# Kernel optimization log

Hardware: AMD Instinct MI355X
Metric: run time of the kernel (lower is better)

Reference implementation:

```python
import math
import jax, jax.numpy as jnp
import numpy as np

EPS_NORM = 1e-6
EPS_COS = 1e-6


def setup_inputs() -> dict:
    key = jax.random.key(0)
    ks = jax.random.split(key, 6)
    B, C, T, H, W = 2, 768, 8, 24, 24
    d_head = 64
    nh = C // d_head  # 12
    x = jax.random.normal(ks[0], (B, C, T, H, W), jnp.float32)
    pos = jax.random.uniform(ks[1], (B, H, W, 2), jnp.float32)
    cond = jax.random.normal(ks[2], (B, C), jnp.float32)
    # NOTE: original zero-inits norm.linear and out_proj; we use small random
    # weights so the reference exercises the full math path.
    norm_w = jax.random.normal(ks[3], (C, C), jnp.float32) * 0.02
    qkv_w = jax.random.normal(ks[4], (3 * C, C), jnp.float32) * (1.0 / math.sqrt(C))
    scale = jnp.full((nh,), 10.0, jnp.float32)
    out_w = jax.random.normal(ks[5], (C, C), jnp.float32) * 0.02
    # AxialRoPE freqs buffer, exactly as in torch:
    dim = d_head // 2
    n = nh * dim // 4
    lf = np.linspace(math.log(math.pi), math.log(10.0 * math.pi), n + 1)[:-1]
    freqs = jnp.asarray(np.exp(lf).reshape(dim // 4, nh).T, jnp.float32)  # [nh, d_head//8]
    return dict(x=x, pos=pos, cond=cond, norm_w=norm_w, qkv_w=qkv_w,
                scale=scale, out_w=out_w, freqs=freqs)


def reference(x, pos, cond, norm_w, qkv_w, scale, out_w, freqs):
    B, C, T, H, W = x.shape
    nh = freqs.shape[0]
    e = C // nh
    s = H * W
    n = B * T
    skip = x

    # b c t h w -> (b t) h w c
    xr = jnp.transpose(x, (0, 2, 3, 4, 1)).reshape(n, H, W, C)
    # cond: b c -> (b t) c
    condr = jnp.repeat(cond, T, axis=0)

    # AdaRMSNorm
    cs = condr @ norm_w.T + 1.0  # [n, C]
    ms = jnp.mean(xr.astype(jnp.float32) ** 2, axis=-1, keepdims=True)
    xn = (xr * (cs[:, None, None, :] * jax.lax.rsqrt(ms + EPS_NORM))).astype(x.dtype)

    # QKV projection
    qkv = xn @ qkv_w.T  # [n, H, W, 3C]
    qkv = qkv.reshape(n, s, 3, nh, e)
    q = jnp.transpose(qkv[:, :, 0], (0, 2, 1, 3))  # [n, nh, s, e]
    k = jnp.transpose(qkv[:, :, 1], (0, 2, 1, 3))
    v = jnp.transpose(qkv[:, :, 2], (0, 2, 1, 3))

    # cosine-sim QK rescale (per-head learned scale)
    sq = jnp.sqrt(scale)[:, None, None]  # [nh,1,1]
    q = q * (sq * jax.lax.rsqrt(jnp.sum(q ** 2, axis=-1, keepdims=True) + EPS_COS))
    k = k * (sq * jax.lax.rsqrt(jnp.sum(k ** 2, axis=-1, keepdims=True) + EPS_COS))

    # axial RoPE: theta [B, s, nh, 2*dth] -> repeat over T -> [n, nh, s, d]
    posf = pos.reshape(B, s, 2)
    th = posf[:, :, 0, None, None] * freqs  # [B, s, nh, dth]
    tw = posf[:, :, 1, None, None] * freqs
    theta = jnp.concatenate([th, tw], axis=-1)
    theta = jnp.repeat(theta, T, axis=0)
    theta = jnp.transpose(theta, (0, 2, 1, 3))  # [n, nh, s, d]
    cos_t, sin_t = jnp.cos(theta), jnp.sin(theta)
    d = theta.shape[-1]

    def rot(t):
        t1, t2, rest = t[..., :d], t[..., d:2 * d], t[..., 2 * d:]
        return jnp.concatenate([t1 * cos_t - t2 * sin_t,
                                t2 * cos_t + t1 * sin_t, rest], axis=-1)

    q = rot(q)
    k = rot(k)

    # SDPA with scale=1.0
    attn = jax.nn.softmax(jnp.einsum('bhqe,bhke->bhqk', q, k), axis=-1)
    o = jnp.einsum('bhqk,bhke->bhqe', attn, v)  # [n, nh, s, e]

    # n nh (h w) e -> n h w (nh e)
    o = jnp.transpose(o, (0, 2, 1, 3)).reshape(n, H, W, C)
    o = o @ out_w.T
    # (b t) h w c -> b c t h w
    o = o.reshape(B, T, H, W, C).transpose(0, 4, 1, 2, 3)
    return o + skip
```

## Files before the change

kernel.cpp:

```cpp
#include <hip/hip_runtime.h>
#include <hip/hip_bf16.h>

#define CDIM 768
#define NHEAD 12
#define EDIM 64
#define TDIM 8
#define SDIM 576
#define NROW 16
#define MDIM 9216
#define QKVN 2304

typedef __attribute__((ext_vector_type(4))) float f32x4;
typedef __bf16 bf16x8 __attribute__((ext_vector_type(8)));
typedef unsigned short u16;
typedef __attribute__((ext_vector_type(8))) unsigned short u16x8;

__device__ inline float bf2f(u16 u) {
  union { unsigned int i; float f; } x; x.i = ((unsigned int)u) << 16; return x.f;
}
__device__ inline u16 f2bf(float f) {
  union { float f; unsigned int i; } x; x.f = f;
  unsigned int i = x.i;
  return (u16)((i + 0x7FFFu + ((i >> 16) & 1u)) >> 16);
}
__device__ inline unsigned cvt_pk_bf16(float lo, float hi) {
  unsigned r;
  asm("v_cvt_pk_bf16_f32 %0, %1, %2" : "=v"(r) : "v"(lo), "v"(hi));
  return r;
}

__global__ __launch_bounds__(256) void prep_kernel(const float* __restrict__ qkv_w,
                                                   u16* __restrict__ wq,
                                                   const float* __restrict__ out_w,
                                                   u16* __restrict__ wo,
                                                   const float* __restrict__ cond,
                                                   const float* __restrict__ nw,
                                                   float* __restrict__ cs,
                                                   const float* __restrict__ pos,
                                                   const float* __restrict__ freqs,
                                                   float2* __restrict__ trig) {
  int bid = blockIdx.x;
  int tid = threadIdx.x;
  if (bid < 1728) {
    int i = bid * 256 + tid;
    float4 v = *(const float4*)(qkv_w + (size_t)i * 4);
    u16* d = wq + (size_t)i * 4;
    d[0] = f2bf(v.x); d[1] = f2bf(v.y); d[2] = f2bf(v.z); d[3] = f2bf(v.w);
  } else if (bid < 2304) {
    int i = (bid - 1728) * 256 + tid;
    float4 v = *(const float4*)(out_w + (size_t)i * 4);
    u16* d = wo + (size_t)i * 4;
    d[0] = f2bf(v.x); d[1] = f2bf(v.y); d[2] = f2bf(v.z); d[3] = f2bf(v.w);
  } else if (bid < 2310) {
    int idx = (bid - 2304) * 256 + tid;
    int b = idx / CDIM, c = idx - b * CDIM;
    const float* cr = cond + (size_t)b * CDIM;
    const float* wr = nw + (size_t)c * CDIM;
    float s = 1.0f;
    for (int j = 0; j < CDIM; j += 4) {
      float4 a = *(const float4*)(cr + j);
      float4 w = *(const float4*)(wr + j);
      s = fmaf(a.x, w.x, s); s = fmaf(a.y, w.y, s);
      s = fmaf(a.z, w.z, s); s = fmaf(a.w, w.w, s);
    }
    cs[idx] = s;
  } else {
    int idx = (bid - 2310) * 256 + tid;
    int j = idx & 15;
    int h = (idx >> 4) % NHEAD;
    int bs = idx / (16 * NHEAD);
    float p = pos[(size_t)bs * 2 + (j >> 3)];
    float th = p * freqs[h * 8 + (j & 7)];
    float sn, cn;
    __sincosf(th, &sn, &cn);
    trig[idx] = make_float2(cn, sn);
  }
}

__global__ __launch_bounds__(256) void norm_kernel(const float* __restrict__ x,
                                                   const float* __restrict__ cs,
                                                   u16* __restrict__ xn) {
  __shared__ float xs[16][772];
  __shared__ float red[16][17];
  __shared__ float rfac[16];
  int n = blockIdx.y;
  int hw0 = blockIdx.x * 16;
  int b = n >> 3, t = n & 7;
  int tx = threadIdx.x, ty = threadIdx.y;
  const float* xb = x + ((size_t)b * CDIM * TDIM + t) * SDIM;
  float acc = 0.0f;
  for (int c = ty; c < CDIM; c += 16) {
    float v = xb[(size_t)c * (TDIM * SDIM) + hw0 + tx];
    xs[tx][c] = v;
    acc = fmaf(v, v, acc);
  }
  red[ty][tx] = acc;
  __syncthreads();
  if (ty == 0) {
    float s = 0.0f;
    #pragma unroll
    for (int j = 0; j < 16; j++) s += red[j][tx];
    rfac[tx] = rsqrtf(s * (1.0f / (float)CDIM) + 1e-6f);
  }
  __syncthreads();
  const float* csb = cs + (size_t)b * CDIM;
  int flat = ty * 16 + tx;
  #pragma unroll
  for (int i = 0; i < 6; i++) {
    int idx = i * 256 + flat;
    int row = idx / 96;
    int cseg = idx - row * 96;
    int c0 = cseg * 8;
    float rf = rfac[row];
    float4 a0 = *(const float4*)&xs[row][c0];
    float4 a1 = *(const float4*)&xs[row][c0 + 4];
    float4 w0 = *(const float4*)(csb + c0);
    float4 w1 = *(const float4*)(csb + c0 + 4);
    u16x8 ov;
    ov[0] = f2bf(a0.x * w0.x * rf); ov[1] = f2bf(a0.y * w0.y * rf);
    ov[2] = f2bf(a0.z * w0.z * rf); ov[3] = f2bf(a0.w * w0.w * rf);
    ov[4] = f2bf(a1.x * w1.x * rf); ov[5] = f2bf(a1.y * w1.y * rf);
    ov[6] = f2bf(a1.z * w1.z * rf); ov[7] = f2bf(a1.w * w1.w * rf);
    *(u16x8*)(xn + ((size_t)n * SDIM + hw0 + row) * CDIM + c0) = ov;
  }
}

__device__ __forceinline__ void gemm_bt_lds(const u16* __restrict__ A,
                                            const u16* __restrict__ B,
                                            int K, int m0, int n0, int tid,
                                            u16* ldsA, u16* ldsB,
                                            f32x4 acc[4][4]) {
  int lane = tid & 63;
  int wid = tid >> 6;
  int wm = (wid >> 1) * 64, wn = (wid & 1) * 64;
  int lr = lane & 15, lg = lane >> 4;
  const u16* gA = A + (size_t)(m0 + wid * 32 + (lane >> 3)) * K + (((lane & 7) ^ (lane >> 3)) * 8);
  const u16* gB = B + (size_t)(n0 + wid * 32 + (lane >> 3)) * K + (((lane & 7) ^ (lane >> 3)) * 8);
  u16* dA = ldsA + wid * 2048;
  u16* dB = ldsB + wid * 2048;
  auto STAGE = [&](int buf, int k0) {
    u16* dAb = dA + buf * 8192;
    u16* dBb = dB + buf * 8192;
    #pragma unroll
    for (int is = 0; is < 4; is++) {
      __builtin_amdgcn_global_load_lds(
          (const __attribute__((address_space(1))) unsigned int*)(gA + (size_t)(is * 8) * K + k0),
          (__attribute__((address_space(3))) unsigned int*)(dAb + is * 512),
          16, 0, 0);
      __builtin_amdgcn_global_load_lds(
          (const __attribute__((address_space(1))) unsigned int*)(gB + (size_t)(is * 8) * K + k0),
          (__attribute__((address_space(3))) unsigned int*)(dBb + is * 512),
          16, 0, 0);
    }
  };
  int nt = K >> 6;
  STAGE(0, 0);
  int cur = 0;
  #pragma unroll 1
  for (int t = 0; t < nt; t++) {
    if (t + 1 < nt) {
      STAGE(cur ^ 1, (t + 1) * 64);
      asm volatile("s_waitcnt vmcnt(8)" ::: "memory");
    } else {
      asm volatile("s_waitcnt vmcnt(0)" ::: "memory");
    }
    __builtin_amdgcn_s_barrier();
    __builtin_amdgcn_sched_barrier(0);
    const u16* lA = ldsA + cur * 8192;
    const u16* lB = ldsB + cur * 8192;
    #pragma unroll
    for (int kk = 0; kk < 2; kk++) {
      bf16x8 af[4], bfr[4];
      #pragma unroll
      for (int i = 0; i < 4; i++)
        af[i]  = *(const bf16x8*)&lA[(wm + i * 16 + lr) * 64 + (((lg + 4 * kk) ^ (lr & 7)) * 8)];
      #pragma unroll
      for (int j = 0; j < 4; j++)
        bfr[j] = *(const bf16x8*)&lB[(wn + j * 16 + lr) * 64 + (((lg + 4 * kk) ^ (lr & 7)) * 8)];
      #pragma unroll
      for (int i = 0; i < 4; i++)
        #pragma unroll
        for (int j = 0; j < 4; j++)
          acc[i][j] = __builtin_amdgcn_mfma_f32_16x16x32_bf16(af[i], bfr[j], acc[i][j], 0, 0, 0);
    }
    __builtin_amdgcn_sched_barrier(0);
    __builtin_amdgcn_s_barrier();
    __builtin_amdgcn_sched_barrier(0);
    cur ^= 1;
  }
}

__device__ __forceinline__ void swz_tile(int L, int& m0, int& n0) {
  int xcd = L & 7, loc = L >> 3;
  int nblk = loc / 9, mloc = loc - nblk * 9;
  m0 = (xcd * 9 + mloc) * 128;
  n0 = nblk * 128;
}

__global__ __launch_bounds__(256) void gemm_qkv(const u16* __restrict__ xn,
                                                const u16* __restrict__ wq,
                                                const float2* __restrict__ trig,
                                                const float* __restrict__ scale,
                                                u16* __restrict__ q,
                                                u16* __restrict__ k,
                                                u16* __restrict__ vt) {
  __shared__ u16 smem[32768];
  u16* ldsA = smem;
  u16* ldsB = smem + 16384;
  f32x4 acc[4][4] = {};
  int tid = threadIdx.x;
  int m0, n0;
  swz_tile(blockIdx.x, m0, n0);
  gemm_bt_lds(xn, wq, CDIM, m0, n0, tid, ldsA, ldsB, acc);
  int lane = tid & 63, wid = tid >> 6;
  int wm = (wid >> 1) * 64, wn = (wid & 1) * 64;
  int lr = lane & 15, rb = (lane >> 4) * 4;
  int part = n0 / CDIM;
  int hbase = (n0 - part * CDIM) >> 6;
  u16* T = smem;
  if (part < 2) {
    int h = hbase + (wn >> 6);
    float sq = sqrtf(scale[h]) * (part == 0 ? 1.44269504f : 1.0f);
    #pragma unroll
    for (int i = 0; i < 4; i++)
      #pragma unroll
      for (int r = 0; r < 4; r++) {
        int m = m0 + wm + i * 16 + rb + r;
        int nidx = m / SDIM, sp = m - nidx * SDIM;
        int b = nidx >> 3;
        float2 cssn = trig[(((size_t)b * SDIM + sp) * NHEAD + h) * 16 + lr];
        float v0 = acc[i][0][r];
        float v1 = acc[i][1][r];
        float v2 = acc[i][2][r];
        float v3 = acc[i][3][r];
        float ss = v0 * v0 + v1 * v1 + v2 * v2 + v3 * v3;
        ss += __shfl_xor(ss, 1); ss += __shfl_xor(ss, 2);
        ss += __shfl_xor(ss, 4); ss += __shfl_xor(ss, 8);
        float rs = sq * rsqrtf(ss + 1e-6f);
        v0 *= rs; v1 *= rs; v2 *= rs; v3 *= rs;
        float o0 = v0 * cssn.x - v1 * cssn.y;
        float o1 = v1 * cssn.x + v0 * cssn.y;
        u16* trow = T + (size_t)(wm + i * 16 + rb + r) * 136 + wn + lr;
        trow[0]  = f2bf(o0); trow[16] = f2bf(o1);
        trow[32] = f2bf(v2); trow[48] = f2bf(v3);
      }
    __syncthreads();
    u16* dst = (part == 0) ? q : k;
    #pragma unroll
    for (int c = 0; c < 8; c++) {
      int chunk = c * 256 + tid;
      int ml = chunk >> 4, sub = chunk & 15;
      int m = m0 + ml;
      int nidx = m / SDIM, sp = m - nidx * SDIM;
      int hl = sub >> 3, e0 = (sub & 7) * 8;
      u16x8 v = *(const u16x8*)&T[(size_t)ml * 136 + sub * 8];
      *(u16x8*)(dst + ((size_t)(nidx * NHEAD + hbase + hl) * SDIM + sp) * EDIM + e0) = v;
    }
  } else {
    #pragma unroll
    for (int i = 0; i < 4; i++)
      #pragma unroll
      for (int j = 0; j < 4; j++)
        #pragma unroll
        for (int r = 0; r < 4; r++)
          T[(size_t)(wn + j * 16 + lr) * 136 + (wm + i * 16 + rb + r)] = f2bf(acc[i][j][r]);
    __syncthreads();
    #pragma unroll
    for (int c = 0; c < 8; c++) {
      int chunk = c * 256 + tid;
      int nl = chunk >> 4, sub = chunk & 15;
      int hl = nl >> 6, e = nl & 63;
      int m = m0 + sub * 8;
      int nidx = m / SDIM, hw = m - nidx * SDIM;
      u16x8 v = *(const u16x8*)&T[(size_t)nl * 136 + sub * 8];
      *(u16x8*)(vt + ((size_t)(nidx * NHEAD + hbase + hl) * EDIM + e) * SDIM + hw) = v;
    }
  }
}

__global__ __launch_bounds__(256, 2) void attn_mfma(const u16* __restrict__ q,
                                                    const u16* __restrict__ k,
                                                    const u16* __restrict__ vt,
                                                    u16* __restrict__ o) {
  __shared__ u16 kbuf[3][4096];
  __shared__ u16 vbuf[3][4096];
  __shared__ u16 p_lds[4][48][72];
  int L = blockIdx.x;
  int cid = (L & 7) * 72 + (L >> 3);
  int nh_ = cid / 3;
  int qt = cid - nh_ * 3;
  int n = nh_ / NHEAD, h = nh_ - n * NHEAD;
  int tid = threadIdx.x;
  int wid = tid >> 6, lane = tid & 63;
  int lr = lane & 15, lg = lane >> 4;
  int qbase = qt * 192 + wid * 48;

  const u16* qp = q + ((size_t)nh_ * SDIM + qbase) * EDIM;
  bf16x8 qa[3][2];
  #pragma unroll
  for (int f = 0; f < 3; f++) {
    qa[f][0] = *(const bf16x8*)(qp + (size_t)(f * 16 + lr) * EDIM + lg * 8);
    qa[f][1] = *(const bf16x8*)(qp + (size_t)(f * 16 + lr) * EDIM + 32 + lg * 8);
  }
  const u16* kb = k + (size_t)nh_ * SDIM * EDIM;
  const u16* vb = vt + (size_t)nh_ * EDIM * SDIM;

  int srow = wid * 16 + (lane >> 3);
  int schunk = (lane & 7) ^ (lane >> 3);
  auto STAGE = [&](int buf, int s0) {
    #pragma unroll
    for (int is = 0; is < 2; is++) {
      int row = srow + is * 8;
      __builtin_amdgcn_global_load_lds(
          (const __attribute__((address_space(1))) unsigned int*)(kb + (size_t)(s0 + row) * EDIM + schunk * 8),
          (__attribute__((address_space(3))) unsigned int*)(&kbuf[buf][(size_t)(wid * 16 + is * 8 + (lane >> 3)) * 64 + (lane & 7) * 8]),
          16, 0, 0);
      __builtin_amdgcn_global_load_lds(
          (const __attribute__((address_space(1))) unsigned int*)(vb + (size_t)row * SDIM + s0 + schunk * 8),
          (__attribute__((address_space(3))) unsigned int*)(&vbuf[buf][(size_t)(wid * 16 + is * 8 + (lane >> 3)) * 64 + (lane & 7) * 8]),
          16, 0, 0);
    }
  };

  float psum[3] = {0.0f, 0.0f, 0.0f};
  f32x4 oacc[3][4] = {};

  STAGE(0, 0);
  STAGE(1, 64);
  #pragma unroll 1
  for (int kt = 0; kt < 9; kt++) {
    if (kt < 8) {
      asm volatile("s_waitcnt vmcnt(4)" ::: "memory");
    } else {
      asm volatile("s_waitcnt vmcnt(0)" ::: "memory");
    }
    __builtin_amdgcn_s_barrier();
    __builtin_amdgcn_sched_barrier(0);
    if (kt < 7) STAGE((kt + 2) % 3, (kt + 2) * 64);
    const u16* kl = kbuf[kt % 3];
    const u16* vl = vbuf[kt % 3];
    bf16x8 kf[4][2];
    #pragma unroll
    for (int j = 0; j < 4; j++) {
      kf[j][0] = *(const bf16x8*)&kl[(j * 16 + lr) * 64 + ((lg       ^ (lr & 7)) * 8)];
      kf[j][1] = *(const bf16x8*)&kl[(j * 16 + lr) * 64 + (((lg + 4) ^ (lr & 7)) * 8)];
    }
    bf16x8 vf[2][4];
    #pragma unroll
    for (int ks = 0; ks < 2; ks++)
      #pragma unroll
      for (int et = 0; et < 4; et++)
        vf[ks][et] = *(const bf16x8*)&vl[(et * 16 + lr) * 64 + (((ks * 4 + lg) ^ (lr & 7)) * 8)];
    #pragma unroll
    for (int f = 0; f < 3; f++) {
      f32x4 sfr[4] = {};
      __builtin_amdgcn_s_setprio(1);
      #pragma unroll
      for (int j = 0; j < 4; j++) {
        sfr[j] = __builtin_amdgcn_mfma_f32_16x16x32_bf16(kf[j][0], qa[f][0], sfr[j], 0, 0, 0);
        sfr[j] = __builtin_amdgcn_mfma_f32_16x16x32_bf16(kf[j][1], qa[f][1], sfr[j], 0, 0, 0);
      }
      __builtin_amdgcn_s_setprio(0);
      float fs = 0.0f;
      #pragma unroll
      for (int j = 0; j < 4; j++) {
        float p0 = exp2f(sfr[j][0]);
        float p1 = exp2f(sfr[j][1]);
        float p2 = exp2f(sfr[j][2]);
        float p3 = exp2f(sfr[j][3]);
        unsigned w0 = cvt_pk_bf16(p0, p1);
        unsigned w1 = cvt_pk_bf16(p2, p3);
        *(unsigned*)&p_lds[wid][f * 16 + lr][j * 16 + lg * 4]     = w0;
        *(unsigned*)&p_lds[wid][f * 16 + lr][j * 16 + lg * 4 + 2] = w1;
        fs += (p0 + p1) + (p2 + p3);
      }
      psum[f] += fs;
    }
    __builtin_amdgcn_s_setprio(1);
    #pragma unroll
    for (int f = 0; f < 3; f++)
      #pragma unroll
      for (int ks = 0; ks < 2; ks++) {
        bf16x8 pa = *(const bf16x8*)&p_lds[wid][f * 16 + lr][ks * 32 + lg * 8];
        #pragma unroll
        for (int et = 0; et < 4; et++)
          oacc[f][et] = __builtin_amdgcn_mfma_f32_16x16x32_bf16(pa, vf[ks][et], oacc[f][et], 0, 0, 0);
      }
    __builtin_amdgcn_s_setprio(0);
    __builtin_amdgcn_sched_barrier(0);
  }
  u16* ob = o + ((size_t)n * SDIM + qbase) * CDIM + h * EDIM;
  #pragma unroll
  for (int f = 0; f < 3; f++) {
    float s = psum[f];
    s += __shfl_xor(s, 16);
    s += __shfl_xor(s, 32);
    float inv = 1.0f / s;
    #pragma unroll
    for (int r = 0; r < 4; r++) {
      float invr = __shfl(inv, lg * 4 + r);
      #pragma unroll
      for (int et = 0; et < 4; et++)
        ob[(size_t)(f * 16 + lg * 4 + r) * CDIM + et * 16 + lr] = f2bf(oacc[f][et][r] * invr);
    }
  }
}

__global__ __launch_bounds__(256) void gemm_proj(const u16* __restrict__ o,
                                                 const u16* __restrict__ wo,
                                                 const float* __restrict__ x,
                                                 float* __restrict__ out) {
  __shared__ __align__(16) char smem[128 * 132 * 4];
  u16* ldsA = (u16*)smem;
  u16* ldsB = (u16*)smem + 16384;
  f32x4 acc[4][4] = {};
  int tid = threadIdx.x;
  int m0, n0;
  swz_tile(blockIdx.x, m0, n0);
  gemm_bt_lds(o, wo, CDIM, m0, n0, tid, ldsA, ldsB, acc);
  int lane = tid & 63, wid = tid >> 6;
  int wm = (wid >> 1) * 64, wn = (wid & 1) * 64;
  int lr = lane & 15, rb = (lane >> 4) * 4;
  float* T = (float*)smem;
  #pragma unroll
  for (int i = 0; i < 4; i++)
    #pragma unroll
    for (int j = 0; j < 4; j++)
      #pragma unroll
      for (int r = 0; r < 4; r++)
        T[(size_t)(wn + j * 16 + lr) * 132 + (wm + i * 16 + rb + r)] = acc[i][j][r];
  __syncthreads();
  #pragma unroll
  for (int c = 0; c < 16; c++) {
    int chunk = c * 256 + tid;
    int nl = chunk >> 5, sub = chunk & 31;
    int m = m0 + sub * 4;
    int nidx = m / SDIM, hw = m - nidx * SDIM;
    int b = nidx >> 3, t = nidx & 7;
    int jj = n0 + nl;
    size_t oi = ((size_t)(b * CDIM + jj) * TDIM + t) * SDIM + hw;
    float4 xv = *(const float4*)&x[oi];
    float4 tv = *(const float4*)&T[(size_t)nl * 132 + sub * 4];
    float4 ov;
    ov.x = tv.x + xv.x; ov.y = tv.y + xv.y;
    ov.z = tv.z + xv.z; ov.w = tv.w + xv.w;
    *(float4*)&out[oi] = ov;
  }
}

extern "C" void kernel_launch(void* const* d_in, const int* in_sizes, int n_in,
                              void* d_out, int out_size, void* d_ws, size_t ws_size,
                              hipStream_t stream) {
  const float* x      = (const float*)d_in[0];
  const float* pos    = (const float*)d_in[1];
  const float* cond   = (const float*)d_in[2];
  const float* norm_w = (const float*)d_in[3];
  const float* qkv_w  = (const float*)d_in[4];
  const float* scale  = (const float*)d_in[5];
  const float* out_w  = (const float*)d_in[6];
  const float* freqs  = (const float*)d_in[7];
  float* out = (float*)d_out;

  char* ws = (char*)d_ws;
  size_t off = 0;
  auto alloc = [&](size_t bytes) -> char* {
    char* p = ws + off;
    off = (off + bytes + 255) & ~(size_t)255;
    return p;
  };
  float* cs   = (float*)alloc(2 * CDIM * sizeof(float));
  u16* wq     = (u16*)alloc((size_t)QKVN * CDIM * 2);
  u16* wo     = (u16*)alloc((size_t)CDIM * CDIM * 2);
  u16* xn     = (u16*)alloc((size_t)MDIM * CDIM * 2);
  u16* qb     = (u16*)alloc((size_t)MDIM * CDIM * 2);
  u16* kb     = (u16*)alloc((size_t)MDIM * CDIM * 2);
  u16* vt     = (u16*)alloc((size_t)MDIM * CDIM * 2);
  u16* ob     = (u16*)alloc((size_t)MDIM * CDIM * 2);
  float2* trg = (float2*)alloc((size_t)2 * SDIM * NHEAD * 16 * sizeof(float2));

  prep_kernel<<<dim3(3174), dim3(256), 0, stream>>>(qkv_w, wq, out_w, wo,
                                                    cond, norm_w, cs, pos, freqs, trg);
  norm_kernel<<<dim3(SDIM / 16, NROW), dim3(16, 16), 0, stream>>>(x, cs, xn);
  gemm_qkv<<<dim3(8 * 9 * (QKVN / 128)), dim3(256), 0, stream>>>(xn, wq, trg, scale, qb, kb, vt);
  attn_mfma<<<dim3(576), dim3(256), 0, stream>>>(qb, kb, vt, ob);
  gemm_proj<<<dim3(8 * 9 * (CDIM / 128)), dim3(256), 0, stream>>>(ob, wo, x, out);
}
```

Baseline: 163.9 us.

## Split cs into tiny kernel and fuse norm with weight casts and trig prep

Moves the cond·norm_w GEMV into its own small kernel so the RMS norm can run inside the same launch as the weight bf16 casts and the RoPE trig table. The weight casts now use packed v_cvt_pk_bf16 with 64-bit stores instead of scalar 16-bit stores. The trig table is transposed to a head-major layout so each block reads contiguous entries. The per-row m/SDIM divisions in the GEMM epilogues are replaced by a compare-and-subtract. The aim is to cut launch count, serialization and per-element overhead, though the 6-block cs kernel still sits serially before the fused launch.

```diff
diff --git a/kernel.cpp b/kernel.cpp
--- a/kernel.cpp
+++ b/kernel.cpp
@@ -29,99 +29,103 @@
   return r;
 }
 
-__global__ __launch_bounds__(256) void prep_kernel(const float* __restrict__ qkv_w,
-                                                   u16* __restrict__ wq,
-                                                   const float* __restrict__ out_w,
-                                                   u16* __restrict__ wo,
-                                                   const float* __restrict__ cond,
-                                                   const float* __restrict__ nw,
-                                                   float* __restrict__ cs,
-                                                   const float* __restrict__ pos,
-                                                   const float* __restrict__ freqs,
-                                                   float2* __restrict__ trig) {
+__global__ __launch_bounds__(256) void cs_kernel(const float* __restrict__ cond,
+                                                 const float* __restrict__ nw,
+                                                 float* __restrict__ cs) {
+  int idx = blockIdx.x * 256 + threadIdx.x;
+  int b = idx / CDIM, c = idx % CDIM;
+  const float* cr = cond + (size_t)b * CDIM;
+  const float* wr = nw + (size_t)c * CDIM;
+  float s = 1.0f;
+  for (int j = 0; j < CDIM; j += 4) {
+    float4 a = *(const float4*)(cr + j);
+    float4 w = *(const float4*)(wr + j);
+    s = fmaf(a.x, w.x, s); s = fmaf(a.y, w.y, s);
+    s = fmaf(a.z, w.z, s); s = fmaf(a.w, w.w, s);
+  }
+  cs[idx] = s;
+}
+
+__global__ __launch_bounds__(256) void norm_prep_kernel(const float* __restrict__ x,
+                                                        const float* __restrict__ cs,
+                                                        u16* __restrict__ xn,
+                                                        const float* __restrict__ qkv_w,
+                                                        u16* __restrict__ wq,
+                                                        const float* __restrict__ out_w,
+                                                        u16* __restrict__ wo,
+                                                        const float* __restrict__ pos,
+                                                        const float* __restrict__ freqs,
+                                                        float2* __restrict__ trig) {
+  __shared__ float xs[16][772];
+  __shared__ float red[16][17];
+  __shared__ float rfac[16];
   int bid = blockIdx.x;
   int tid = threadIdx.x;
-  if (bid < 1728) {
-    int i = bid * 256 + tid;
+  if (bid < 576) {
+    int n = bid / 36;
+    int hw0 = (bid - n * 36) * 16;
+    int b = n >> 3, t = n & 7;
+    int tx = tid & 15, ty = tid >> 4;
+    const float* xb = x + ((size_t)b * CDIM * TDIM + t) * SDIM;
+    float acc = 0.0f;
+    for (int c = ty; c < CDIM; c += 16) {
+      float v = xb[(size_t)c * (TDIM * SDIM) + hw0 + tx];
+      xs[tx][c] = v;
+      acc = fmaf(v, v, acc);
+    }
+    red[ty][tx] = acc;
+    __syncthreads();
+    if (ty == 0) {
+      float s = 0.0f;
+      #pragma unroll
+      for (int j = 0; j < 16; j++) s += red[j][tx];
+      rfac[tx] = rsqrtf(s * (1.0f / (float)CDIM) + 1e-6f);
+    }
+    __syncthreads();
+    const float* csb = cs + (size_t)b * CDIM;
+    #pragma unroll
+    for (int i = 0; i < 6; i++) {
+      int idx = i * 256 + tid;
+      int row = idx / 96;
+      int cseg = idx - row * 96;
+      int c0 = cseg * 8;
+      float rf = rfac[row];
+      float4 a0 = *(const float4*)&xs[row][c0];
+      float4 a1 = *(const float4*)&xs[row][c0 + 4];
+      float4 w0 = *(const float4*)(csb + c0);
+      float4 w1 = *(const float4*)(csb + c0 + 4);
+      union { u16x8 v; unsigned u[4]; } ov;
+      ov.u[0] = cvt_pk_bf16(a0.x * w0.x * rf, a0.y * w0.y * rf);
+      ov.u[1] = cvt_pk_bf16(a0.z * w0.z * rf, a0.w * w0.w * rf);
+      ov.u[2] = cvt_pk_bf16(a1.x * w1.x * rf, a1.y * w1.y * rf);
+      ov.u[3] = cvt_pk_bf16(a1.z * w1.z * rf, a1.w * w1.w * rf);
+      *(u16x8*)(xn + ((size_t)n * SDIM + hw0 + row) * CDIM + c0) = ov.v;
+    }
+  } else if (bid < 2304) {
+    int i = (bid - 576) * 256 + tid;
     float4 v = *(const float4*)(qkv_w + (size_t)i * 4);
-    u16* d = wq + (size_t)i * 4;
-    d[0] = f2bf(v.x); d[1] = f2bf(v.y); d[2] = f2bf(v.z); d[3] = f2bf(v.w);
-  } else if (bid < 2304) {
-    int i = (bid - 1728) * 256 + tid;
+    union { unsigned long long d; unsigned u[2]; } pk;
+    pk.u[0] = cvt_pk_bf16(v.x, v.y);
+    pk.u[1] = cvt_pk_bf16(v.z, v.w);
+    *(unsigned long long*)(wq + (size_t)i * 4) = pk.d;
+  } else if (bid < 2880) {
+    int i = (bid - 2304) * 256 + tid;
     float4 v = *(const float4*)(out_w + (size_t)i * 4);
-    u16* d = wo + (size_t)i * 4;
-    d[0] = f2bf(v.x); d[1] = f2bf(v.y); d[2] = f2bf(v.z); d[3] = f2bf(v.w);
-  } else if (bid < 2310) {
-    int idx = (bid - 2304) * 256 + tid;
-    int b = idx / CDIM, c = idx - b * CDIM;
-    const float* cr = cond + (size_t)b * CDIM;
-    const float* wr = nw + (size_t)c * CDIM;
-    float s = 1.0f;
-    for (int j = 0; j < CDIM; j += 4) {
-      float4 a = *(const float4*)(cr + j);
-      float4 w = *(const float4*)(wr + j);
-      s = fmaf(a.x, w.x, s); s = fmaf(a.y, w.y, s);
-      s = fmaf(a.z, w.z, s); s = fmaf(a.w, w.w, s);
-    }
-    cs[idx] = s;
+    union { unsigned long long d; unsigned u[2]; } pk;
+    pk.u[0] = cvt_pk_bf16(v.x, v.y);
+    pk.u[1] = cvt_pk_bf16(v.z, v.w);
+    *(unsigned long long*)(wo + (size_t)i * 4) = pk.d;
   } else {
-    int idx = (bid - 2310) * 256 + tid;
+    int idx = (bid - 2880) * 256 + tid;
     int j = idx & 15;
-    int h = (idx >> 4) % NHEAD;
-    int bs = idx / (16 * NHEAD);
+    int hb = idx >> 4;
+    int h = hb / 1152;
+    int bs = hb - h * 1152;
     float p = pos[(size_t)bs * 2 + (j >> 3)];
     float th = p * freqs[h * 8 + (j & 7)];
     float sn, cn;
     __sincosf(th, &sn, &cn);
     trig[idx] = make_float2(cn, sn);
-  }
-}
-
-__global__ __launch_bounds__(256) void norm_kernel(const float* __restrict__ x,
-                                                   const float* __restrict__ cs,
-                                                   u16* __restrict__ xn) {
-  __shared__ float xs[16][772];
-  __shared__ float red[16][17];
-  __shared__ float rfac[16];
-  int n = blockIdx.y;
-  int hw0 = blockIdx.x * 16;
-  int b = n >> 3, t = n & 7;
-  int tx = threadIdx.x, ty = threadIdx.y;
-  const float* xb = x + ((size_t)b * CDIM * TDIM + t) * SDIM;
-  float acc = 0.0f;
-  for (int c = ty; c < CDIM; c += 16) {
-    float v = xb[(size_t)c * (TDIM * SDIM) + hw0 + tx];
-    xs[tx][c] = v;
-    acc = fmaf(v, v, acc);
-  }
-  red[ty][tx] = acc;
-  __syncthreads();
-  if (ty == 0) {
-    float s = 0.0f;
-    #pragma unroll
-    for (int j = 0; j < 16; j++) s += red[j][tx];
-    rfac[tx] = rsqrtf(s * (1.0f / (float)CDIM) + 1e-6f);
-  }
-  __syncthreads();
-  const float* csb = cs + (size_t)b * CDIM;
-  int flat = ty * 16 + tx;
-  #pragma unroll
-  for (int i = 0; i < 6; i++) {
-    int idx = i * 256 + flat;
-    int row = idx / 96;
-    int cseg = idx - row * 96;
-    int c0 = cseg * 8;
-    float rf = rfac[row];
-    float4 a0 = *(const float4*)&xs[row][c0];
-    float4 a1 = *(const float4*)&xs[row][c0 + 4];
-    float4 w0 = *(const float4*)(csb + c0);
-    float4 w1 = *(const float4*)(csb + c0 + 4);
-    u16x8 ov;
-    ov[0] = f2bf(a0.x * w0.x * rf); ov[1] = f2bf(a0.y * w0.y * rf);
-    ov[2] = f2bf(a0.z * w0.z * rf); ov[3] = f2bf(a0.w * w0.w * rf);
-    ov[4] = f2bf(a1.x * w1.x * rf); ov[5] = f2bf(a1.y * w1.y * rf);
-    ov[6] = f2bf(a1.z * w1.z * rf); ov[7] = f2bf(a1.w * w1.w * rf);
-    *(u16x8*)(xn + ((size_t)n * SDIM + hw0 + row) * CDIM + c0) = ov;
   }
 }
 
@@ -217,18 +221,22 @@
   int lr = lane & 15, rb = (lane >> 4) * 4;
   int part = n0 / CDIM;
   int hbase = (n0 - part * CDIM) >> 6;
+  int nidx_b = m0 / SDIM, rm0 = m0 - nidx_b * SDIM;
   u16* T = smem;
   if (part < 2) {
     int h = hbase + (wn >> 6);
     float sq = sqrtf(scale[h]) * (part == 0 ? 1.44269504f : 1.0f);
+    const float2* tg = trig + (size_t)h * 1152 * 16;
     #pragma unroll
     for (int i = 0; i < 4; i++)
       #pragma unroll
       for (int r = 0; r < 4; r++) {
-        int m = m0 + wm + i * 16 + rb + r;
-        int nidx = m / SDIM, sp = m - nidx * SDIM;
+        int off = wm + i * 16 + rb + r;
+        int sp = rm0 + off;
+        int nidx = nidx_b + (sp >= SDIM);
+        sp -= (sp >= SDIM) ? SDIM : 0;
         int b = nidx >> 3;
-        float2 cssn = trig[(((size_t)b * SDIM + sp) * NHEAD + h) * 16 + lr];
+        float2 cssn = tg[((size_t)b * SDIM + sp) * 16 + lr];
         float v0 = acc[i][0][r];
         float v1 = acc[i][1][r];
         float v2 = acc[i][2][r];
@@ -240,7 +248,7 @@
         v0 *= rs; v1 *= rs; v2 *= rs; v3 *= rs;
         float o0 = v0 * cssn.x - v1 * cssn.y;
         float o1 = v1 * cssn.x + v0 * cssn.y;
-        u16* trow = T + (size_t)(wm + i * 16 + rb + r) * 136 + wn + lr;
+        u16* trow = T + (size_t)off * 136 + wn + lr;
         trow[0]  = f2bf(o0); trow[16] = f2bf(o1);
         trow[32] = f2bf(v2); trow[48] = f2bf(v3);
       }
@@ -250,8 +258,9 @@
     for (int c = 0; c < 8; c++) {
       int chunk = c * 256 + tid;
       int ml = chunk >> 4, sub = chunk & 15;
-      int m = m0 + ml;
-      int nidx = m / SDIM, sp = m - nidx * SDIM;
+      int sp = rm0 + ml;
+      int nidx = nidx_b + (sp >= SDIM);
+      sp -= (sp >= SDIM) ? SDIM : 0;
       int hl = sub >> 3, e0 = (sub & 7) * 8;
       u16x8 v = *(const u16x8*)&T[(size_t)ml * 136 + sub * 8];
       *(u16x8*)(dst + ((size_t)(nidx * NHEAD + hbase + hl) * SDIM + sp) * EDIM + e0) = v;
@@ -270,8 +279,9 @@
       int chunk = c * 256 + tid;
       int nl = chunk >> 4, sub = chunk & 15;
       int hl = nl >> 6, e = nl & 63;
-      int m = m0 + sub * 8;
-      int nidx = m / SDIM, hw = m - nidx * SDIM;
+      int hw = rm0 + sub * 8;
+      int nidx = nidx_b + (hw >= SDIM);
+      hw -= (hw >= SDIM) ? SDIM : 0;
       u16x8 v = *(const u16x8*)&T[(size_t)nl * 136 + sub * 8];
       *(u16x8*)(vt + ((size_t)(nidx * NHEAD + hbase + hl) * EDIM + e) * SDIM + hw) = v;
     }
@@ -421,6 +431,7 @@
   int lane = tid & 63, wid = tid >> 6;
   int wm = (wid >> 1) * 64, wn = (wid & 1) * 64;
   int lr = lane & 15, rb = (lane >> 4) * 4;
+  int nidx_b = m0 / SDIM, rm0 = m0 - nidx_b * SDIM;
   float* T = (float*)smem;
   #pragma unroll
   for (int i = 0; i < 4; i++)
@@ -434,8 +445,9 @@
   for (int c = 0; c < 16; c++) {
     int chunk = c * 256 + tid;
     int nl = chunk >> 5, sub = chunk & 31;
-    int m = m0 + sub * 4;
-    int nidx = m / SDIM, hw = m - nidx * SDIM;
+    int hw = rm0 + sub * 4;
+    int nidx = nidx_b + (hw >= SDIM);
+    hw -= (hw >= SDIM) ? SDIM : 0;
     int b = nidx >> 3, t = nidx & 7;
     int jj = n0 + nl;
     size_t oi = ((size_t)(b * CDIM + jj) * TDIM + t) * SDIM + hw;
@@ -476,11 +488,11 @@
   u16* kb     = (u16*)alloc((size_t)MDIM * CDIM * 2);
   u16* vt     = (u16*)alloc((size_t)MDIM * CDIM * 2);
   u16* ob     = (u16*)alloc((size_t)MDIM * CDIM * 2);
-  float2* trg = (float2*)alloc((size_t)2 * SDIM * NHEAD * 16 * sizeof(float2));
-
-  prep_kernel<<<dim3(3174), dim3(256), 0, stream>>>(qkv_w, wq, out_w, wo,
-                                                    cond, norm_w, cs, pos, freqs, trg);
-  norm_kernel<<<dim3(SDIM / 16, NROW), dim3(16, 16), 0, stream>>>(x, cs, xn);
+  float2* trg = (float2*)alloc((size_t)NHEAD * 2 * SDIM * 16 * sizeof(float2));
+
+  cs_kernel<<<dim3(6), dim3(256), 0, stream>>>(cond, norm_w, cs);
+  norm_prep_kernel<<<dim3(3744), dim3(256), 0, stream>>>(x, cs, xn, qkv_w, wq,
+                                                         out_w, wo, pos, freqs, trg);
   gemm_qkv<<<dim3(8 * 9 * (QKVN / 128)), dim3(256), 0, stream>>>(xn, wq, trg, scale, qb, kb, vt);
   attn_mfma<<<dim3(576), dim3(256), 0, stream>>>(qb, kb, vt, ob);
   gemm_proj<<<dim3(8 * 9 * (CDIM / 128)), dim3(256), 0, stream>>>(ob, wo, x, out);
```

Result: no change. 161.9 us (-1.2%).
